# Kernel optimization log

Measured on AMD Instinct MI355X. Metric: run time of the kernel, lower is better.

The kernel has to match this reference:

```python
import jax, jax.numpy as jnp
import numpy as np

# Deterministic stand-ins for the torch RNG draws in the original forward
# (rot sampled from {0,40,...,320}, shifts from [-20,20], flips from {2,3}).
ROT_DEG = 40.0          # rotations[1]
SHIFTS = (5, -7)        # roll shifts on (H, W)
FLIP_DIMS = (2, 3)      # flip W and D dims (torch.arange(2,4) both selected)


def _rotate_nn_maps(H, W, deg):
    """Nearest-neighbor inverse-rotation index maps for an HxW grid
    (matches torchvision rotate: nearest interp, expand=False, fill=0)."""
    theta = jnp.deg2rad(jnp.float32(deg))
    cy = (H - 1) / 2.0
    cx = (W - 1) / 2.0
    i = jnp.arange(H, dtype=jnp.float32)[:, None] - cy  # [H,1]
    j = jnp.arange(W, dtype=jnp.float32)[None, :] - cx  # [1,W]
    c, s = jnp.cos(theta), jnp.sin(theta)
    # inverse rotation: map each output pixel back to its source location
    src_i = c * i + s * j + cy
    src_j = -s * i + c * j + cx
    si = jnp.round(src_i).astype(jnp.int32)
    sj = jnp.round(src_j).astype(jnp.int32)
    valid = (si >= 0) & (si < H) & (sj >= 0) & (sj < W)
    return jnp.clip(si, 0, H - 1), jnp.clip(sj, 0, W - 1), valid


def setup_inputs() -> dict:
    key = jax.random.key(0)
    features = jax.random.normal(key, (16, 128, 128, 8, 16), dtype=jnp.float32)
    return {"features": features}


def reference(features):
    # features: [B, H, W, D, F]; one fused gather rotates the (H, W) plane for
    # every (sample, depth, feature) simultaneously, replacing the original
    # per-(sample, feature) Python rotate() loop.
    B, H, W, D, F = features.shape
    si, sj, valid = _rotate_nn_maps(H, W, ROT_DEG)
    rotated = jnp.where(valid[None, :, :, None, None],
                        features[:, si, sj, :, :], 0.0)  # [B,H,W,D,F]
    rolled = jnp.roll(rotated, SHIFTS, axis=(1, 2))
    flipped = jnp.flip(rolled, axis=FLIP_DIMS)
    return flipped
```

## Files before the change

kernel.cpp:

```cpp
#include <hip/hip_runtime.h>
#include <math.h>

#define BB 16
#define HH 128
#define WW 128
#define DD 8
#define FF 16


typedef float floatx4 __attribute__((ext_vector_type(4)));

__global__ __launch_bounds__(256) void aug_kernel(const floatx4* __restrict__ in,
                                                  floatx4* __restrict__ out) {
    int t = blockIdx.x * blockDim.x + threadIdx.x;
    int f4 = t & 3;   t >>= 2;
    int d  = t & 7;   t >>= 3;
    int w  = t & 127; t >>= 7;
    int h  = t;

    int i = (h + 123) & 127;
    int j = (134 - w) & 127;

    const double c = 0.76604444311897803;
    const double s = 0.64278760968653933;
    const double cy = 63.5, cx = 63.5;
    double di = (double)i - cy;
    double dj = (double)j - cx;
    int si = (int)rint(c * di + s * dj + cy);
    int sj = (int)rint(-s * di + c * dj + cx);
    bool valid = (si >= 0) & (si < HH) & (sj >= 0) & (sj < WW);

    const int STRIDE = HH * WW * DD * (FF / 4);
    int out0 = ((h * WW + w) * DD + d) * 4 + f4;

    if (valid) {
        int dd = 7 - d;
        int src0 = ((si * WW + sj) * DD + dd) * 4 + f4;
        #pragma unroll
        for (int b = 0; b < BB; ++b) {
            floatx4 v = in[src0 + b * STRIDE];
            __builtin_nontemporal_store(v, &out[out0 + b * STRIDE]);
        }
    } else {
        floatx4 z = (floatx4)(0.f);
        #pragma unroll
        for (int b = 0; b < BB; ++b) {
            __builtin_nontemporal_store(z, &out[out0 + b * STRIDE]);
        }
    }
}

extern "C" void kernel_launch(void* const* d_in, const int* in_sizes, int n_in,
                              void* d_out, int out_size, void* d_ws, size_t ws_size,
                              hipStream_t stream) {
    const floatx4* in = (const floatx4*)d_in[0];
    floatx4* out = (floatx4*)d_out;
    int n_threads = HH * WW * DD * (FF / 4);
    int block = 256;
    int grid = n_threads / block;
    aug_kernel<<<grid, block, 0, stream>>>(in, out);
}
```

Before: 235.4 us.

## Map one vec4 per thread and swizzle blocks across XCDs

Instead of each thread looping over all 16 batch samples, every thread now handles a single float4 with the batch index decoded from its global id. This multiplies the grid by 16. Block ids are remapped so that the blocks landing on each of the 8 XCDs cover a contiguous chunk of the output, which should improve L2 locality for the gathered reads. The cost is more address arithmetic per element, and the double-precision rotation maths is now recomputed for every batch sample.

```diff
diff --git a/kernel.cpp b/kernel.cpp
--- a/kernel.cpp
+++ b/kernel.cpp
@@ -12,11 +12,18 @@
 
 __global__ __launch_bounds__(256) void aug_kernel(const floatx4* __restrict__ in,
                                                   floatx4* __restrict__ out) {
-    int t = blockIdx.x * blockDim.x + threadIdx.x;
+    const int NB  = (BB * HH * WW * DD * (FF / 4)) / 256;
+    const int CPX = NB / 8;
+    int bid = blockIdx.x;
+    int sb  = (bid & 7) * CPX + (bid >> 3);
+    int tid = sb * 256 + (int)threadIdx.x;
+
+    int t  = tid;
     int f4 = t & 3;   t >>= 2;
     int d  = t & 7;   t >>= 3;
     int w  = t & 127; t >>= 7;
-    int h  = t;
+    int h  = t & 127; t >>= 7;
+    int b  = t;
 
     int i = (h + 123) & 127;
     int j = (134 - w) & 127;
@@ -30,24 +37,13 @@
     int sj = (int)rint(-s * di + c * dj + cx);
     bool valid = (si >= 0) & (si < HH) & (sj >= 0) & (sj < WW);
 
-    const int STRIDE = HH * WW * DD * (FF / 4);
-    int out0 = ((h * WW + w) * DD + d) * 4 + f4;
-
+    floatx4 v = (floatx4)(0.f);
     if (valid) {
         int dd = 7 - d;
-        int src0 = ((si * WW + sj) * DD + dd) * 4 + f4;
-        #pragma unroll
-        for (int b = 0; b < BB; ++b) {
-            floatx4 v = in[src0 + b * STRIDE];
-            __builtin_nontemporal_store(v, &out[out0 + b * STRIDE]);
-        }
-    } else {
-        floatx4 z = (floatx4)(0.f);
-        #pragma unroll
-        for (int b = 0; b < BB; ++b) {
-            __builtin_nontemporal_store(z, &out[out0 + b * STRIDE]);
-        }
+        int src = ((((b * HH) + si) * WW + sj) * DD + dd) * 4 + f4;
+        v = in[src];
     }
+    __builtin_nontemporal_store(v, &out[tid]);
 }
 
 extern "C" void kernel_launch(void* const* d_in, const int* in_sizes, int n_in,
@@ -55,8 +51,8 @@
                               hipStream_t stream) {
     const floatx4* in = (const floatx4*)d_in[0];
     floatx4* out = (floatx4*)d_out;
-    int n_threads = HH * WW * DD * (FF / 4);
+    int n_vec4 = out_size / 4;
     int block = 256;
-    int grid = n_threads / block;
+    int grid = n_vec4 / block;
     aug_kernel<<<grid, block, 0, stream>>>(in, out);
 }
```

After: 224.2 us. 1.05x faster.
